# Performance work log

Measured on AMD Instinct MI355X. Metric: run time of the kernel, lower is better.

The kernel has to match this reference:

```python
import jax, jax.numpy as jnp
import numpy as np

EPS = 1e-5
PATCH_SIZES = [None, 13]
PATCH_WEIGHTS = [0.5, 0.5]


def _box(x, p):
    # sliding-window sum over spatial dims, VALID padding -> [B,C,H-p+1,W-p+1]
    return jax.lax.reduce_window(x, 0.0, jax.lax.add, (1, 1, p, p), (1, 1, 1, 1), 'VALID')


def _global_ncc(x1, x2):
    # InstanceNorm2d (biased var, eps) per (b,c) over spatial dims, then dot / (c*h*w)
    b, c, h, w = x1.shape
    m1 = jnp.mean(x1, axis=(2, 3), keepdims=True)
    m2 = jnp.mean(x2, axis=(2, 3), keepdims=True)
    v1 = jnp.mean((x1 - m1) ** 2, axis=(2, 3), keepdims=True)
    v2 = jnp.mean((x2 - m2) ** 2, axis=(2, 3), keepdims=True)
    n1 = (x1 - m1) * jax.lax.rsqrt(v1 + EPS)
    n2 = (x2 - m2) * jax.lax.rsqrt(v2 + EPS)
    return jnp.sum(n1 * n2, axis=(1, 2, 3)) / (c * h * w)


def _patch_ncc(x1, x2, p):
    # Equivalent fused form of: unfold -> rearrange (patch locations become
    # channels, pxp patch pixels become spatial) -> InstanceNorm2d -> dot.
    # Each pxp patch is normalized over its own pixels => local NCC.
    b, c, h, w = x1.shape
    n = p * p
    s1 = _box(x1, p)
    s2 = _box(x2, p)
    s11 = _box(x1 * x1, p)
    s22 = _box(x2 * x2, p)
    s12 = _box(x1 * x2, p)
    m1 = s1 / n
    m2 = s2 / n
    v1 = s11 / n - m1 * m1  # biased variance, matches InstanceNorm2d
    v2 = s22 / n - m2 * m2
    cross = s12 - n * m1 * m2  # sum_p (I-mI)(J-mJ)
    cc = cross * jax.lax.rsqrt((v1 + EPS) * (v2 + EPS))  # [B,C,H',W']
    hp, wp = h - p + 1, w - p + 1
    # original divides by (channels' * h' * w') where channels' = c*hp*wp, spatial = p*p
    return jnp.sum(cc, axis=(1, 2, 3)) / (c * hp * wp * n)


def setup_inputs() -> dict:
    key = jax.random.key(0)
    k1, k2 = jax.random.split(key)
    x1 = jax.random.normal(k1, (32, 1, 512, 512), dtype=jnp.float32)
    x2 = jax.random.normal(k2, (32, 1, 512, 512), dtype=jnp.float32)
    return {"x1": x1, "x2": x2}


def reference(x1, x2):
    scores = []
    for w, p in zip(PATCH_WEIGHTS, PATCH_SIZES):
        if p is None:
            scores.append(w * _global_ncc(x1, x2))
        else:
            scores.append(w * _patch_ncc(x1, x2, p))
    return jnp.stack(scores, axis=0).sum(axis=0)  # [B]
```

## Files before the change

### kernel.cpp

```cpp
#include <hip/hip_runtime.h>

#define EPS 1e-5f

typedef float v2f __attribute__((ext_vector_type(2)));

constexpr int B = 32;
constexpr int H = 512;
constexpr int W = 512;
constexpr int NPIX = H * W;
constexpr int P = 13;
constexpr int HP = H - P + 1;
constexpr int WP = W - P + 1;
constexpr int TILES_X = 8;
constexpr int BAND_OUT = 27;
constexpr int BANDS_Y = 19;
constexpr int G = 13;
constexpr int NGROUPS = 3;
constexpr int BLOCKS_PER_B = TILES_X * BANDS_Y;
constexpr int ROWF = 80;

#define GLOAD_LDS16(gp, lp)                                                    \
  __builtin_amdgcn_global_load_lds(                                            \
      (const __attribute__((address_space(1))) unsigned int*)(const void*)(gp),\
      (__attribute__((address_space(3))) unsigned int*)(void*)(lp), 16, 0, 0)

__global__ __launch_bounds__(64) void ncc_fused_kernel(
    const float* __restrict__ x1, const float* __restrict__ x2,
    float* __restrict__ part) {
  const int bid = blockIdx.x;
  const int b    = bid / BLOCKS_PER_B;
  const int rem  = bid % BLOCKS_PER_B;
  const int tile = rem % TILES_X;
  const int band = rem / TILES_X;
  const bool last = (band == BANDS_Y - 1);
  const int x0 = tile * 64;
  const int y0 = last ? (HP - BAND_OUT) : band * BAND_OUT;
  const int tid = threadIdx.x;
  const bool valid = (x0 + tid) < WP;

  __shared__ float sa[2][G][ROWF];
  __shared__ float sb[2][G][ROWF];

  const float* r1 = x1 + (size_t)b * NPIX + (size_t)y0 * W + x0;
  const float* r2 = x2 + (size_t)b * NPIX + (size_t)y0 * W + x0;

  int qoff = tid * 4;
  { int mx = W - x0 - 4; if (qoff > mx) qoff = mx; }
  const bool loader = tid < 19;

  auto stage = [&](int g, int buf) {
    if (loader) {
#pragma unroll
      for (int r = 0; r < G; ++r) {
        GLOAD_LDS16(r1 + (size_t)(g * G + r) * W + qoff, &sa[buf][r][0]);
        GLOAD_LDS16(r2 + (size_t)(g * G + r) * W + qoff, &sb[buf][r][0]);
      }
    }
  };

  float rh1[G], rh2[G], rh11[G], rh22[G], rh12[G];
  float S1 = 0.f, S2 = 0.f, S11 = 0.f, S22 = 0.f, S12 = 0.f;
  float g1 = 0.f, g2 = 0.f, g11 = 0.f, g22 = 0.f, g12 = 0.f;
  float acc = 0.f;
  const float inv_n = 1.0f / 169.0f;

  auto step = [&](int u, int buf, int t, bool fill) {
    const float* pa = &sa[buf][u][tid];
    const float* pb = &sb[buf][u][tid];
    v2f va[6], vb[6];
#pragma unroll
    for (int k = 0; k < 6; ++k) {
      va[k].x = pa[2 * k];     va[k].y = pa[2 * k + 1];
      vb[k].x = pb[2 * k];     vb[k].y = pb[2 * k + 1];
    }
    float a12 = pa[12], b12 = pb[12];

    v2f h1v = va[0], h2v = vb[0];
    v2f h11v = va[0] * va[0], h22v = vb[0] * vb[0], h12v = va[0] * vb[0];
#pragma unroll
    for (int k = 1; k < 6; ++k) {
      h1v += va[k];
      h2v += vb[k];
      h11v += va[k] * va[k];
      h22v += vb[k] * vb[k];
      h12v += va[k] * vb[k];
    }
    float h1 = h1v.x + h1v.y + a12;
    float h2 = h2v.x + h2v.y + b12;
    float h11 = fmaf(a12, a12, h11v.x + h11v.y);
    float h22 = fmaf(b12, b12, h22v.x + h22v.y);
    float h12 = fmaf(a12, b12, h12v.x + h12v.y);

    bool owned = last ? (t >= G) : (t < BAND_OUT);
    if (owned) {
      float a0 = va[0].x, b0 = vb[0].x;
      g1 += a0; g2 += b0;
      g11 = fmaf(a0, a0, g11);
      g22 = fmaf(b0, b0, g22);
      g12 = fmaf(a0, b0, g12);
    }

    if (fill) {
      S1 += h1; S2 += h2; S11 += h11; S22 += h22; S12 += h12;
    } else {
      S1 += h1 - rh1[u]; S2 += h2 - rh2[u];
      S11 += h11 - rh11[u]; S22 += h22 - rh22[u]; S12 += h12 - rh12[u];
    }
    rh1[u] = h1; rh2[u] = h2; rh11[u] = h11; rh22[u] = h22; rh12[u] = h12;

    if (t >= 12 && (!last || t >= 25)) {
      float m1 = S1 * inv_n, m2 = S2 * inv_n;
      float vv1 = fmaf(-m1, m1, S11 * inv_n) + EPS;
      float vv2 = fmaf(-m2, m2, S22 * inv_n) + EPS;
      float cross = fmaf(-S1 * inv_n, S2, S12);
      float cc = cross * rsqrtf(vv1 * vv2);
      acc += valid ? cc : 0.f;
    }
  };

  stage(0, 0);
  __syncthreads();
  stage(1, 1);

#pragma unroll
  for (int u = 0; u < G; ++u) step(u, 0, u, true);
  __syncthreads();

#pragma clang loop unroll(disable)
  for (int g = 1; g < NGROUPS; ++g) {
    if (g + 1 < NGROUPS) stage(g + 1, (g + 1) & 1);
    const int buf = g & 1;
#pragma unroll
    for (int u = 0; u < G; ++u) step(u, buf, g * G + u, false);
    __syncthreads();
  }

  float v0 = acc, v1 = g1, v2 = g2, v3 = g11, v4 = g22, v5 = g12;
#pragma unroll
  for (int off = 32; off > 0; off >>= 1) {
    v0 += __shfl_down(v0, off, 64);
    v1 += __shfl_down(v1, off, 64);
    v2 += __shfl_down(v2, off, 64);
    v3 += __shfl_down(v3, off, 64);
    v4 += __shfl_down(v4, off, 64);
    v5 += __shfl_down(v5, off, 64);
  }
  if (tid == 0) {
    float* o = part + (size_t)bid * 6;
    o[0] = v0; o[1] = v1; o[2] = v2; o[3] = v3; o[4] = v4; o[5] = v5;
  }
}

__global__ __launch_bounds__(64) void final_kernel(
    const float* __restrict__ part, float* __restrict__ out) {
  int b = blockIdx.x;
  int tid = threadIdx.x;
  float s[6] = {0.f, 0.f, 0.f, 0.f, 0.f, 0.f};
  for (int i = tid; i < BLOCKS_PER_B; i += 64) {
    const float* p = part + (size_t)(b * BLOCKS_PER_B + i) * 6;
#pragma unroll
    for (int k = 0; k < 6; ++k) s[k] += p[k];
  }
#pragma unroll
  for (int off = 32; off > 0; off >>= 1) {
#pragma unroll
    for (int k = 0; k < 6; ++k) s[k] += __shfl_down(s[k], off, 64);
  }
  if (tid == 0) {
    float Nf = (float)NPIX;
    float m1 = s[1] / Nf;
    float m2 = s[2] / Nf;
    float v1 = fmaf(-m1, m1, s[3] / Nf);
    float v2 = fmaf(-m2, m2, s[4] / Nf);
    float cross = fmaf(-Nf * m1, m2, s[5]);
    float g = cross * rsqrtf((v1 + EPS) * (v2 + EPS)) / Nf;
    float patch = s[0] / ((float)HP * (float)WP * 169.0f);
    out[b] = 0.5f * g + 0.5f * patch;
  }
}

extern "C" void kernel_launch(void* const* d_in, const int* in_sizes, int n_in,
                              void* d_out, int out_size, void* d_ws, size_t ws_size,
                              hipStream_t stream) {
  const float* x1 = (const float*)d_in[0];
  const float* x2 = (const float*)d_in[1];
  float* out = (float*)d_out;
  float* part = (float*)d_ws;

  ncc_fused_kernel<<<B * BLOCKS_PER_B, 64, 0, stream>>>(x1, x2, part);
  final_kernel<<<B, 64, 0, stream>>>(part, out);
}
```

Measured before the change: 126.3 us.

## Compute two adjacent output columns per thread with wider tiles and taller bands

Each thread now produces two neighbouring output columns. The second column's horizontal 13-tap sums are derived from the first by subtracting one pixel and adding one, and all state is held in 2-wide float vectors. Tiles widen to 128 columns and bands grow to 40 output rows across 4 row groups, which cuts the overlapping halo loads and the redundant horizontal sums. The cost is more registers per thread and fewer blocks in the grid, which may lower occupancy.

After: 122.3 us. -3.2%, faster.

```diff
diff --git a/kernel.cpp b/kernel.cpp
--- a/kernel.cpp
+++ b/kernel.cpp
@@ -11,13 +11,15 @@
 constexpr int P = 13;
 constexpr int HP = H - P + 1;
 constexpr int WP = W - P + 1;
-constexpr int TILES_X = 8;
-constexpr int BAND_OUT = 27;
-constexpr int BANDS_Y = 19;
+constexpr int TILES_X = 4;
+constexpr int BAND_OUT = 40;
+constexpr int BANDS_Y = 13;
 constexpr int G = 13;
-constexpr int NGROUPS = 3;
+constexpr int NGROUPS = 4;
+constexpr int ITER_LAST_OWN = 20;
+constexpr int ITER_LAST_EMIT = 32;
 constexpr int BLOCKS_PER_B = TILES_X * BANDS_Y;
-constexpr int ROWF = 80;
+constexpr int RS = 140;
 
 #define GLOAD_LDS16(gp, lp)                                                    \
   __builtin_amdgcn_global_load_lds(                                            \
@@ -33,20 +35,22 @@
   const int tile = rem % TILES_X;
   const int band = rem / TILES_X;
   const bool last = (band == BANDS_Y - 1);
-  const int x0 = tile * 64;
+  const int x0 = tile * 128;
   const int y0 = last ? (HP - BAND_OUT) : band * BAND_OUT;
   const int tid = threadIdx.x;
-  const bool valid = (x0 + tid) < WP;
-
-  __shared__ float sa[2][G][ROWF];
-  __shared__ float sb[2][G][ROWF];
+  const int c0 = x0 + 2 * tid;
+  const bool valid0 = c0 < WP;
+  const bool valid1 = (c0 + 1) < WP;
+
+  __shared__ float sa[2][G][RS];
+  __shared__ float sb[2][G][RS];
 
   const float* r1 = x1 + (size_t)b * NPIX + (size_t)y0 * W + x0;
   const float* r2 = x2 + (size_t)b * NPIX + (size_t)y0 * W + x0;
 
   int qoff = tid * 4;
   { int mx = W - x0 - 4; if (qoff > mx) qoff = mx; }
-  const bool loader = tid < 19;
+  const bool loader = tid < 35;
 
   auto stage = [&](int g, int buf) {
     if (loader) {
@@ -58,63 +62,69 @@
     }
   };
 
-  float rh1[G], rh2[G], rh11[G], rh22[G], rh12[G];
-  float S1 = 0.f, S2 = 0.f, S11 = 0.f, S22 = 0.f, S12 = 0.f;
-  float g1 = 0.f, g2 = 0.f, g11 = 0.f, g22 = 0.f, g12 = 0.f;
+  v2f rr1[G], rr2[G], rr11[G], rr22[G], rr12[G];
+  v2f S1 = {0.f, 0.f}, S2 = {0.f, 0.f}, S11 = {0.f, 0.f}, S22 = {0.f, 0.f},
+      S12 = {0.f, 0.f};
+  v2f g1 = {0.f, 0.f}, g2 = {0.f, 0.f}, g11 = {0.f, 0.f}, g22 = {0.f, 0.f},
+      g12 = {0.f, 0.f};
   float acc = 0.f;
   const float inv_n = 1.0f / 169.0f;
 
   auto step = [&](int u, int buf, int t, bool fill) {
-    const float* pa = &sa[buf][u][tid];
-    const float* pb = &sb[buf][u][tid];
-    v2f va[6], vb[6];
-#pragma unroll
-    for (int k = 0; k < 6; ++k) {
-      va[k].x = pa[2 * k];     va[k].y = pa[2 * k + 1];
-      vb[k].x = pb[2 * k];     vb[k].y = pb[2 * k + 1];
-    }
-    float a12 = pa[12], b12 = pb[12];
-
-    v2f h1v = va[0], h2v = vb[0];
-    v2f h11v = va[0] * va[0], h22v = vb[0] * vb[0], h12v = va[0] * vb[0];
+    const float* pa = &sa[buf][u][2 * tid];
+    const float* pb = &sb[buf][u][2 * tid];
+    v2f A[7], Bv[7];
+#pragma unroll
+    for (int k = 0; k < 7; ++k) {
+      A[k] = *(const v2f*)(pa + 2 * k);
+      Bv[k] = *(const v2f*)(pb + 2 * k);
+    }
+
+    v2f q11 = A[0] * A[0], q22 = Bv[0] * Bv[0], q12 = A[0] * Bv[0];
+    v2f h1v = A[0], h2v = Bv[0], h11v = q11, h22v = q22, h12v = q12;
 #pragma unroll
     for (int k = 1; k < 6; ++k) {
-      h1v += va[k];
-      h2v += vb[k];
-      h11v += va[k] * va[k];
-      h22v += vb[k] * vb[k];
-      h12v += va[k] * vb[k];
-    }
-    float h1 = h1v.x + h1v.y + a12;
-    float h2 = h2v.x + h2v.y + b12;
-    float h11 = fmaf(a12, a12, h11v.x + h11v.y);
-    float h22 = fmaf(b12, b12, h22v.x + h22v.y);
-    float h12 = fmaf(a12, b12, h12v.x + h12v.y);
-
-    bool owned = last ? (t >= G) : (t < BAND_OUT);
+      h1v += A[k];
+      h2v += Bv[k];
+      h11v += A[k] * A[k];
+      h22v += Bv[k] * Bv[k];
+      h12v += A[k] * Bv[k];
+    }
+    float a12 = A[6].x, b12 = Bv[6].x, a13 = A[6].y, b13 = Bv[6].y;
+    float h1_0 = h1v.x + h1v.y + a12;
+    float h2_0 = h2v.x + h2v.y + b12;
+    float h11_0 = fmaf(a12, a12, h11v.x + h11v.y);
+    float h22_0 = fmaf(b12, b12, h22v.x + h22v.y);
+    float h12_0 = fmaf(a12, b12, h12v.x + h12v.y);
+    v2f h1 = {h1_0, h1_0 - A[0].x + a13};
+    v2f h2 = {h2_0, h2_0 - Bv[0].x + b13};
+    v2f h11 = {h11_0, fmaf(a13, a13, h11_0 - q11.x)};
+    v2f h22 = {h22_0, fmaf(b13, b13, h22_0 - q22.x)};
+    v2f h12 = {h12_0, fmaf(a13, b13, h12_0 - q12.x)};
+
+    bool owned = last ? (t >= ITER_LAST_OWN) : (t < BAND_OUT);
     if (owned) {
-      float a0 = va[0].x, b0 = vb[0].x;
-      g1 += a0; g2 += b0;
-      g11 = fmaf(a0, a0, g11);
-      g22 = fmaf(b0, b0, g22);
-      g12 = fmaf(a0, b0, g12);
+      g1 += A[0]; g2 += Bv[0]; g11 += q11; g22 += q22; g12 += q12;
     }
 
     if (fill) {
       S1 += h1; S2 += h2; S11 += h11; S22 += h22; S12 += h12;
     } else {
-      S1 += h1 - rh1[u]; S2 += h2 - rh2[u];
-      S11 += h11 - rh11[u]; S22 += h22 - rh22[u]; S12 += h12 - rh12[u];
-    }
-    rh1[u] = h1; rh2[u] = h2; rh11[u] = h11; rh22[u] = h22; rh12[u] = h12;
-
-    if (t >= 12 && (!last || t >= 25)) {
-      float m1 = S1 * inv_n, m2 = S2 * inv_n;
-      float vv1 = fmaf(-m1, m1, S11 * inv_n) + EPS;
-      float vv2 = fmaf(-m2, m2, S22 * inv_n) + EPS;
-      float cross = fmaf(-S1 * inv_n, S2, S12);
-      float cc = cross * rsqrtf(vv1 * vv2);
-      acc += valid ? cc : 0.f;
+      S1 += h1 - rr1[u]; S2 += h2 - rr2[u];
+      S11 += h11 - rr11[u]; S22 += h22 - rr22[u]; S12 += h12 - rr12[u];
+    }
+    rr1[u] = h1; rr2[u] = h2; rr11[u] = h11; rr22[u] = h22; rr12[u] = h12;
+
+    bool do_out = (t >= 12) && (!last || t >= ITER_LAST_EMIT);
+    if (do_out) {
+      v2f m1 = S1 * inv_n, m2 = S2 * inv_n;
+      v2f vv1 = S11 * inv_n - m1 * m1 + EPS;
+      v2f vv2 = S22 * inv_n - m2 * m2 + EPS;
+      v2f cross = S12 - (S1 * inv_n) * S2;
+      v2f den = vv1 * vv2;
+      float cc0 = cross.x * rsqrtf(den.x);
+      float cc1 = cross.y * rsqrtf(den.y);
+      acc += (valid0 ? cc0 : 0.f) + (valid1 ? cc1 : 0.f);
     }
   };
 
@@ -135,19 +145,21 @@
     __syncthreads();
   }
 
-  float v0 = acc, v1 = g1, v2 = g2, v3 = g11, v4 = g22, v5 = g12;
+  float v0 = acc;
+  float w1 = g1.x + g1.y, w2 = g2.x + g2.y;
+  float w3 = g11.x + g11.y, w4 = g22.x + g22.y, w5 = g12.x + g12.y;
 #pragma unroll
   for (int off = 32; off > 0; off >>= 1) {
     v0 += __shfl_down(v0, off, 64);
-    v1 += __shfl_down(v1, off, 64);
-    v2 += __shfl_down(v2, off, 64);
-    v3 += __shfl_down(v3, off, 64);
-    v4 += __shfl_down(v4, off, 64);
-    v5 += __shfl_down(v5, off, 64);
+    w1 += __shfl_down(w1, off, 64);
+    w2 += __shfl_down(w2, off, 64);
+    w3 += __shfl_down(w3, off, 64);
+    w4 += __shfl_down(w4, off, 64);
+    w5 += __shfl_down(w5, off, 64);
   }
   if (tid == 0) {
     float* o = part + (size_t)bid * 6;
-    o[0] = v0; o[1] = v1; o[2] = v2; o[3] = v3; o[4] = v4; o[5] = v5;
+    o[0] = v0; o[1] = w1; o[2] = w2; o[3] = w3; o[4] = w4; o[5] = w5;
   }
 }
 
```
